# Kernel optimization log

Measured on AMD Instinct MI355X. Metric: run time of the kernel, lower is better.

## Reference

```python
import jax, jax.numpy as jnp
import numpy as np
import math

B, S, D, H = 4, 1024, 512, 8
HD = D // H
HID = 4 * D


def clinear(xr, xi, lm, ph, bm=None, bp=None):
    # magnitude-phase parameterized complex linear: W = exp(lm) * e^{i*ph}
    mag = jnp.exp(lm)
    wr = mag * jnp.cos(ph)
    wi = mag * jnp.sin(ph)
    r = xr @ wr.T - xi @ wi.T
    i = xr @ wi.T + xi @ wr.T
    if bm is not None:
        r = r + bm * jnp.cos(bp)
        i = i + bm * jnp.sin(bp)
    return r, i


def cln(xr, xi, gr, gi, br, bi, eps=1e-6):
    mr = xr.mean(-1, keepdims=True)
    mi = xi.mean(-1, keepdims=True)
    cr, ci = xr - mr, xi - mi
    var = (cr * cr + ci * ci).mean(-1, keepdims=True)
    inv = 1.0 / jnp.sqrt(var + eps)
    nr, ni = cr * inv, ci * inv
    return nr * gr - ni * gi + br, nr * gi + ni * gr + bi


def rotate_half(x):
    h = x.shape[-1] // 2
    return jnp.concatenate([-x[..., h:], x[..., :h]], axis=-1)


def split_heads(x):  # (B,S,D) -> (B,H,S,HD)
    return x.reshape(B, S, H, HD).transpose(0, 2, 1, 3)


def merge_heads(x):  # (B,H,S,HD) -> (B,S,D)
    return x.transpose(0, 2, 1, 3).reshape(B, S, D)


def setup_inputs() -> dict:
    key = jax.random.key(0)
    ks = iter(jax.random.split(key, 64))

    def lin(o_f, i_f):
        lm = jax.random.normal(next(ks), (o_f, i_f)) * 0.1 - 0.5 * math.log(i_f)
        ph = jax.random.uniform(next(ks), (o_f, i_f), minval=-math.pi, maxval=math.pi)
        return lm.astype(jnp.float32), ph.astype(jnp.float32)

    inp = {}
    inp['x_real'] = jax.random.normal(next(ks), (B, S, D), dtype=jnp.float32)
    inp['x_imag'] = jax.random.normal(next(ks), (B, S, D), dtype=jnp.float32)
    inp['ln1_gr'] = jnp.ones(D); inp['ln1_gi'] = jnp.zeros(D)
    inp['ln1_br'] = jnp.zeros(D); inp['ln1_bi'] = jnp.zeros(D)
    for nm in ['q', 'k', 'v', 'o']:
        lm, ph = lin(D, D)
        inp[nm + '_lm'] = lm; inp[nm + '_ph'] = ph
        inp[nm + '_bm'] = jnp.zeros(D); inp[nm + '_bp'] = jnp.zeros(D)
    inp['ln2_gr'] = jnp.ones(D); inp['ln2_gi'] = jnp.zeros(D)
    inp['ln2_br'] = jnp.zeros(D); inp['ln2_bi'] = jnp.zeros(D)
    inp['gate_lm'], inp['gate_ph'] = lin(HID, D)
    inp['up_lm'], inp['up_ph'] = lin(HID, D)
    inp['down_lm'], inp['down_ph'] = lin(D, HID)
    return inp


def reference(x_real, x_imag, ln1_gr, ln1_gi, ln1_br, ln1_bi,
              q_lm, q_ph, q_bm, q_bp, k_lm, k_ph, k_bm, k_bp,
              v_lm, v_ph, v_bm, v_bp, o_lm, o_ph, o_bm, o_bp,
              ln2_gr, ln2_gi, ln2_br, ln2_bi,
              gate_lm, gate_ph, up_lm, up_ph, down_lm, down_ph):
    # --- pre-attention complex LayerNorm ---
    hr, hi = cln(x_real, x_imag, ln1_gr, ln1_gi, ln1_br, ln1_bi)

    # --- complex QKV projections ---
    qr, qi = clinear(hr, hi, q_lm, q_ph, q_bm, q_bp)
    kr, ki = clinear(hr, hi, k_lm, k_ph, k_bm, k_bp)
    vr, vi = clinear(hr, hi, v_lm, v_ph, v_bm, v_bp)
    qr, qi = split_heads(qr), split_heads(qi)
    kr, ki = split_heads(kr), split_heads(ki)
    vr, vi = split_heads(vr), split_heads(vi)

    # --- complex RoPE (same real rotation applied to real & imag parts) ---
    pos = jnp.arange(S, dtype=jnp.float32)
    inv_freq = 1.0 / (10000.0 ** (jnp.arange(0, HD, 2, dtype=jnp.float32) / HD))
    freqs = pos[:, None] * inv_freq[None, :]          # (S, HD/2)
    cos = jnp.concatenate([jnp.cos(freqs)] * 2, -1)[None, None]  # (1,1,S,HD)
    sin = jnp.concatenate([jnp.sin(freqs)] * 2, -1)[None, None]
    rot = lambda x: x * cos + rotate_half(x) * sin
    qr, qi, kr, ki = rot(qr), rot(qi), rot(kr), rot(ki)

    # --- Hermitian attention: Re(q . conj(k)) = qr.kr + qi.ki ---
    scale = 1.0 / math.sqrt(HD)
    scores = (jnp.einsum('bhqd,bhkd->bhqk', qr, kr)
              + jnp.einsum('bhqd,bhkd->bhqk', qi, ki)) * scale
    causal = jnp.tril(jnp.ones((S, S), dtype=bool))
    scores = jnp.where(causal, scores, jnp.float32(-1e9))
    attn = jax.nn.softmax(scores, axis=-1)            # real-valued weights
    ar = jnp.einsum('bhqk,bhkd->bhqd', attn, vr)
    ai = jnp.einsum('bhqk,bhkd->bhqd', attn, vi)
    ar, ai = merge_heads(ar), merge_heads(ai)
    ar, ai = clinear(ar, ai, o_lm, o_ph, o_bm, o_bp)

    # --- residual + LN2 ---
    res_r, res_i = x_real + ar, x_imag + ai
    hr, hi = cln(res_r, res_i, ln2_gr, ln2_gi, ln2_br, ln2_bi)

    # --- complex gated FFN (SwiGLU-style, complex gating) ---
    gr_, gi_ = clinear(hr, hi, gate_lm, gate_ph)
    s = jax.nn.sigmoid(jnp.sqrt(gr_ * gr_ + gi_ * gi_))  # sigmoid(|gate|)
    gar, gai = gr_ * s, gi_ * s
    ur, ui = clinear(hr, hi, up_lm, up_ph)
    hid_r = gar * ur - gai * ui
    hid_i = gar * ui + gai * ur
    dr, di = clinear(hid_r, hid_i, down_lm, down_ph)

    out_r = res_r + dr
    out_i = res_i + di
    return jnp.stack([out_r, out_i], axis=0)  # (2, B, S, D)
```

## Files before the change

kernel.cpp:

```cpp
#include <hip/hip_runtime.h>
#include <math.h>

#define kB 4
#define kS 1024
#define kD 512
#define kH 8
#define kHD 64
#define kHID 2048
#define kNT (kB * kS)
#define kBSD (kNT * kD)

typedef __attribute__((ext_vector_type(8))) short bf16x8;
typedef __attribute__((ext_vector_type(4))) float f32x4;

#define AS1 __attribute__((address_space(1)))
#define AS3 __attribute__((address_space(3)))

__device__ __forceinline__ float bf2f(unsigned short u) {
  return __uint_as_float(((unsigned int)u) << 16);
}
__device__ __forceinline__ unsigned short f2bf(float f) {
  unsigned int u = __float_as_uint(f);
  u += 0x7fffu + ((u >> 16) & 1u);
  return (unsigned short)(u >> 16);
}
__device__ __forceinline__ unsigned int pack2(unsigned short a, unsigned short b) {
  return (unsigned)a | ((unsigned)b << 16);
}

__global__ __launch_bounds__(256) void build_wA_kernel(
    const float* __restrict__ qlm, const float* __restrict__ qph,
    const float* __restrict__ klm, const float* __restrict__ kph,
    const float* __restrict__ vlm, const float* __restrict__ vph,
    const float* __restrict__ olm, const float* __restrict__ oph,
    const float* __restrict__ qbm, const float* __restrict__ qbp,
    const float* __restrict__ kbm, const float* __restrict__ kbp,
    const float* __restrict__ vbm, const float* __restrict__ vbp,
    const float* __restrict__ obm, const float* __restrict__ obp,
    const float* __restrict__ xr, const float* __restrict__ xi,
    const float* __restrict__ g_r, const float* __restrict__ g_i,
    const float* __restrict__ b_r, const float* __restrict__ b_i,
    unsigned short* __restrict__ Wqkv, unsigned short* __restrict__ Wo,
    float* __restrict__ qkvBias, float* __restrict__ oBias,
    unsigned short* __restrict__ H) {
  int bx = blockIdx.x;
  if (bx >= 4104) {
    int w = threadIdx.x >> 6, lane = threadIdx.x & 63;
    int t = (bx - 4104) * 4 + w;
    int d0 = lane * 8;
    const float* xrt = xr + (size_t)t * 512 + d0;
    const float* xit = xi + (size_t)t * 512 + d0;
    float4 a0 = *(const float4*)&xrt[0];
    float4 a1 = *(const float4*)&xrt[4];
    float4 c0 = *(const float4*)&xit[0];
    float4 c1 = *(const float4*)&xit[4];
    float s1 = a0.x + a0.y + a0.z + a0.w + a1.x + a1.y + a1.z + a1.w;
    float s2 = c0.x + c0.y + c0.z + c0.w + c1.x + c1.y + c1.z + c1.w;
#pragma unroll
    for (int off = 1; off < 64; off <<= 1) {
      s1 += __shfl_xor(s1, off);
      s2 += __shfl_xor(s2, off);
    }
    float mr = s1 * (1.f / kD), mi = s2 * (1.f / kD);
    float ar[8] = {a0.x, a0.y, a0.z, a0.w, a1.x, a1.y, a1.z, a1.w};
    float ai[8] = {c0.x, c0.y, c0.z, c0.w, c1.x, c1.y, c1.z, c1.w};
    float v = 0.f;
#pragma unroll
    for (int e = 0; e < 8; e++) {
      float cr = ar[e] - mr, ci = ai[e] - mi;
      v += cr * cr + ci * ci;
    }
#pragma unroll
    for (int off = 1; off < 64; off <<= 1) v += __shfl_xor(v, off);
    float inv = rsqrtf(v * (1.f / kD) + 1e-6f);
    unsigned short pr[8], pi[8];
#pragma unroll
    for (int e = 0; e < 8; e++) {
      float nr = (ar[e] - mr) * inv;
      float ni = (ai[e] - mi) * inv;
      pr[e] = f2bf(nr * g_r[d0 + e] - ni * g_i[d0 + e] + b_r[d0 + e]);
      pi[e] = f2bf(nr * g_i[d0 + e] + ni * g_r[d0 + e] + b_i[d0 + e]);
    }
    unsigned short* ot = H + (size_t)t * 1024 + d0;
    *(bf16x8*)&ot[0] = *(const bf16x8*)pr;
    *(bf16x8*)&ot[512] = *(const bf16x8*)pi;
    return;
  }
  if (bx >= 4096) {
    int gid = (bx - 4096) * 256 + threadIdx.x;
    int seg = gid >> 9, m = gid & 511;
    const float* bm = seg == 0 ? qbm : seg == 1 ? kbm : seg == 2 ? vbm : obm;
    const float* bp = seg == 0 ? qbp : seg == 1 ? kbp : seg == 2 ? vbp : obp;
    float s, c;
    __sincosf(bp[m], &s, &c);
    float br = bm[m] * c, bi = bm[m] * s;
    if (seg < 3) {
      int h = m >> 6, d = m & 63;
      qkvBias[seg * 1024 + h * 128 + d] = br;
      qkvBias[seg * 1024 + h * 128 + 64 + d] = bi;
    } else {
      oBias[m] = br;
      oBias[512 + m] = bi;
    }
    return;
  }
  int gid = bx * 256 + threadIdx.x;
  int seg = gid >> 18;
  int id = gid & 262143;
  const float* lm = seg == 0 ? qlm : seg == 1 ? klm : seg == 2 ? vlm : olm;
  const float* ph = seg == 0 ? qph : seg == 1 ? kph : seg == 2 ? vph : oph;
  float mm = __expf(lm[id]);
  float s, c;
  __sincosf(ph[id], &s, &c);
  float wr = mm * c, wi = mm * s;
  int m = id >> 9, k = id & 511;
  if (seg < 3) {
    int h = m >> 6, d = m & 63;
    size_t rowR = (size_t)seg * 1024 + h * 128 + d;
    size_t rowI = rowR + 64;
    Wqkv[rowR * 1024 + k] = f2bf(wr);
    Wqkv[rowR * 1024 + 512 + k] = f2bf(-wi);
    Wqkv[rowI * 1024 + k] = f2bf(wi);
    Wqkv[rowI * 1024 + 512 + k] = f2bf(wr);
  } else {
    Wo[(size_t)m * 1024 + k] = f2bf(wr);
    Wo[(size_t)m * 1024 + 512 + k] = f2bf(-wi);
    Wo[(size_t)(512 + m) * 1024 + k] = f2bf(wi);
    Wo[(size_t)(512 + m) * 1024 + 512 + k] = f2bf(wr);
  }
}

__global__ __launch_bounds__(256) void build_wB_kernel(
    const float* __restrict__ glm, const float* __restrict__ gph,
    const float* __restrict__ ulm, const float* __restrict__ uph,
    const float* __restrict__ dlm, const float* __restrict__ dph,
    unsigned short* __restrict__ Wgu, unsigned short* __restrict__ Wd) {
  int gid = blockIdx.x * 256 + threadIdx.x;
  int seg = gid >> 19;
  int id0 = (gid & 524287) * 2;
  const float* lm = seg == 0 ? glm : seg == 1 ? ulm : dlm;
  const float* ph = seg == 0 ? gph : seg == 1 ? uph : dph;
  float2 lm2 = *(const float2*)&lm[id0];
  float2 ph2 = *(const float2*)&ph[id0];
  float m0 = __expf(lm2.x), m1 = __expf(lm2.y);
  float s0, c0, s1, c1;
  __sincosf(ph2.x, &s0, &c0);
  __sincosf(ph2.y, &s1, &c1);
  float wr0 = m0 * c0, wi0 = m0 * s0;
  float wr1 = m1 * c1, wi1 = m1 * s1;
  if (seg < 2) {
    int T = id0 >> 9, k = id0 & 511;
    size_t base = (size_t)(T >> 4) * 64 + (T & 15);
    size_t rR = base + (seg * 2 + 0) * 16;
    size_t rI = base + (seg * 2 + 1) * 16;
    *(unsigned int*)&Wgu[rR * 1024 + k] = pack2(f2bf(wr0), f2bf(wr1));
    *(unsigned int*)&Wgu[rR * 1024 + 512 + k] = pack2(f2bf(-wi0), f2bf(-wi1));
    *(unsigned int*)&Wgu[rI * 1024 + k] = pack2(f2bf(wi0), f2bf(wi1));
    *(unsigned int*)&Wgu[rI * 1024 + 512 + k] = pack2(f2bf(wr0), f2bf(wr1));
  } else {
    int m = id0 >> 11, j = id0 & 2047;
    ushort4 a;
    a.x = f2bf(wr0); a.y = f2bf(-wi0); a.z = f2bf(wr1); a.w = f2bf(-wi1);
    *(ushort4*)&Wd[(size_t)m * 4096 + 2 * j] = a;
    ushort4 b;
    b.x = f2bf(wi0); b.y = f2bf(wr0); b.z = f2bf(wi1); b.w = f2bf(wr1);
    *(ushort4*)&Wd[(size_t)(512 + m) * 4096 + 2 * j] = b;
  }
}

__global__ __launch_bounds__(256) void cln_kernel(
    const float* __restrict__ xr, const float* __restrict__ xi, int stride,
    const float* __restrict__ g_r, const float* __restrict__ g_i,
    const float* __restrict__ b_r, const float* __restrict__ b_i,
    unsigned short* __restrict__ out) {
  int w = threadIdx.x >> 6, lane = threadIdx.x & 63;
  int t = blockIdx.x * 4 + w;
  int d0 = lane * 8;
  const float* xrt = xr + (size_t)t * stride + d0;
  const float* xit = xi + (size_t)t * stride + d0;
  float4 a0 = *(const float4*)&xrt[0];
  float4 a1 = *(const float4*)&xrt[4];
  float4 c0 = *(const float4*)&xit[0];
  float4 c1 = *(const float4*)&xit[4];

  float s1 = a0.x + a0.y + a0.z + a0.w + a1.x + a1.y + a1.z + a1.w;
  float s2 = c0.x + c0.y + c0.z + c0.w + c1.x + c1.y + c1.z + c1.w;
#pragma unroll
  for (int off = 1; off < 64; off <<= 1) {
    s1 += __shfl_xor(s1, off);
    s2 += __shfl_xor(s2, off);
  }
  float mr = s1 * (1.f / kD), mi = s2 * (1.f / kD);

  float ar[8] = {a0.x, a0.y, a0.z, a0.w, a1.x, a1.y, a1.z, a1.w};
  float ai[8] = {c0.x, c0.y, c0.z, c0.w, c1.x, c1.y, c1.z, c1.w};
  float v = 0.f;
#pragma unroll
  for (int e = 0; e < 8; e++) {
    float cr = ar[e] - mr, ci = ai[e] - mi;
    v += cr * cr + ci * ci;
  }
#pragma unroll
  for (int off = 1; off < 64; off <<= 1) v += __shfl_xor(v, off);
  float inv = rsqrtf(v * (1.f / kD) + 1e-6f);

  unsigned short pr[8], pi[8];
#pragma unroll
  for (int e = 0; e < 8; e++) {
    float nr = (ar[e] - mr) * inv;
    float ni = (ai[e] - mi) * inv;
    pr[e] = f2bf(nr * g_r[d0 + e] - ni * g_i[d0 + e] + b_r[d0 + e]);
    pi[e] = f2bf(nr * g_i[d0 + e] + ni * g_r[d0 + e] + b_i[d0 + e]);
  }
  unsigned short* ot = out + (size_t)t * 1024 + d0;
  *(bf16x8*)&ot[0] = *(const bf16x8*)pr;
  *(bf16x8*)&ot[512] = *(const bf16x8*)pi;
}

__global__ __launch_bounds__(256) void cgemm_mfma_kernel(
    const unsigned short* __restrict__ X, int ldx,
    const unsigned short* __restrict__ Wt, int K,
    const float* __restrict__ bias, int mode,
    unsigned short* __restrict__ outb, int ldo,
    unsigned short* __restrict__ vtb) {
  __shared__ unsigned short Sh[128 * 64 * 2];
  unsigned short* Xs = Sh;
  unsigned short* Ws = Sh + 8192;

  const int tid = threadIdx.x;
  const int w = tid >> 6;
  const int lane = tid & 63;
  const int quad = lane >> 4;
  const int l15 = lane & 15;
  const int m0 = blockIdx.x * 128;
  const int n0 = blockIdx.y * 128;
  const int wm = (w & 1) * 64;
  const int wn = (w >> 1) * 64;

  const int rsub = lane >> 3;
  const int grow = w * 32 + rsub;
  const int gcol = ((lane & 7) ^ rsub) * 8;
  const unsigned short* gx = X + (size_t)(n0 + grow) * ldx + gcol;
  const unsigned short* gw = Wt + (size_t)(m0 + grow) * K + gcol;

  const int rg = (l15 & 7);

  f32x4 acc[4][4];
#pragma unroll
  for (int i = 0; i < 4; i++)
#pragma unroll
    for (int j = 0; j < 4; j++) acc[i][j] = (f32x4){0.f, 0.f, 0.f, 0.f};

  for (int k0 = 0; k0 < K; k0 += 64) {
    __syncthreads();
#pragma unroll
    for (int t = 0; t < 4; t++) {
      __builtin_amdgcn_global_load_lds((const AS1 void*)(gx + (size_t)t * 8 * ldx + k0),
                                       (AS3 void*)&Xs[w * 2048 + t * 512], 16, 0, 0);
      __builtin_amdgcn_global_load_lds((const AS1 void*)(gw + (size_t)t * 8 * K + k0),
                                       (AS3 void*)&Ws[w * 2048 + t * 512], 16, 0, 0);
    }
    __syncthreads();

#pragma unroll
    for (int ks = 0; ks < 2; ks++) {
      const int gsel = ((ks * 4 + quad) ^ rg) * 8;
      bf16x8 af[4], bf[4];
#pragma unroll
      for (int t = 0; t < 4; t++) {
        af[t] = *(const bf16x8*)&Xs[(wn + t * 16 + l15) * 64 + gsel];
        bf[t] = *(const bf16x8*)&Ws[(wm + t * 16 + l15) * 64 + gsel];
      }
#pragma unroll
      for (int i = 0; i < 4; i++)
#pragma unroll
        for (int j = 0; j < 4; j++)
          acc[i][j] = __builtin_amdgcn_mfma_f32_16x16x32_bf16(af[i], bf[j], acc[i][j], 0, 0, 0);
    }
  }

  if (mode == 4) {
    int T = ((m0 + wm) >> 6) * 16 + l15;
#pragma unroll
    for (int i = 0; i < 4; ++i) {
      int row0 = n0 + wn + i * 16 + quad * 4;
#pragma unroll
      for (int r = 0; r < 4; ++r) {
        float gr = acc[i][0][r], gi = acc[i][1][r];
        float ur = acc[i][2][r], ui = acc[i][3][r];
        float sg = __builtin_amdgcn_rcpf(1.f + __expf(-sqrtf(gr * gr + gi * gi)));
        float gar = gr * sg, gai = gi * sg;
        unsigned int pk = pack2(f2bf(gar * ur - gai * ui), f2bf(gar * ui + gai * ur));
        *(unsigned int*)&outb[(size_t)(row0 + r) * ldo + 2 * T] = pk;
      }
    }
  } else if (mode == 3 && m0 < 2048) {
#pragma unroll
    for (int j = 0; j < 4; ++j) {
      float bv = bias[m0 + wm + j * 16 + l15];
#pragma unroll
      for (int i = 0; i < 4; ++i)
#pragma unroll
        for (int r = 0; r < 4; ++r) acc[i][j][r] += bv;
    }
    const int sbase = ((n0 + wn) & (kS - 1)) + quad * 4;
#pragma unroll
    for (int j01 = 0; j01 < 2; ++j01) {
      float fi = (float)(j01 * 16 + l15);
      float f = __expf(fi * -0.28782313662425572f);
      float c1, s1, c16, s16, cI, sI;
      __sincosf(f, &s1, &c1);
      __sincosf(16.f * f, &s16, &c16);
      __sincosf((float)sbase * f, &sI, &cI);
#pragma unroll
      for (int i = 0; i < 4; ++i) {
        float cc = cI, ss = sI;
#pragma unroll
        for (int r = 0; r < 4; ++r) {
          float x0 = acc[i][j01][r], x1 = acc[i][j01 + 2][r];
          acc[i][j01][r] = x0 * cc - x1 * ss;
          acc[i][j01 + 2][r] = x1 * cc + x0 * ss;
          float cn = cc * c1 - ss * s1;
          ss = ss * c1 + cc * s1;
          cc = cn;
        }
        float cn = cI * c16 - sI * s16;
        sI = sI * c16 + cI * s16;
        cI = cn;
      }
    }
#pragma unroll
    for (int j = 0; j < 4; ++j) {
      int col = m0 + wm + j * 16 + l15;
#pragma unroll
      for (int i = 0; i < 4; ++i) {
        int row0 = n0 + wn + i * 16 + quad * 4;
#pragma unroll
        for (int r = 0; r < 4; ++r)
          outb[(size_t)(row0 + r) * ldo + col] = f2bf(acc[i][j][r]);
      }
    }
  } else {
    unsigned short* Ts = Sh;
#pragma unroll
    for (int p = 0; p < 2; ++p) {
      __syncthreads();
      if ((w & 1) == p) {
#pragma unroll
        for (int j = 0; j < 4; ++j) {
          float bv = bias[m0 + wm + j * 16 + l15];
          int fl = j * 16 + l15;
#pragma unroll
          for (int i = 0; i < 4; ++i) {
            int tk = wn + i * 16 + quad * 4;
#pragma unroll
            for (int r = 0; r < 4; ++r)
              Ts[fl * 130 + tk + r] = f2bf(acc[i][j][r] + bv);
          }
        }
      }
      __syncthreads();
      {
        int fr = tid >> 2, seg = tid & 3;
        int f = (m0 - 2048) + p * 64 + fr;
        int hh = f >> 7, dc = f & 127;
        int bb = n0 >> 10, sbase2 = (n0 & (kS - 1)) + seg * 32;
        unsigned short* dst = &vtb[(size_t)((bb * 8 + hh) * 128 + dc) * 1024 + sbase2];
        const unsigned short* src = &Ts[fr * 130 + seg * 32];
#pragma unroll
        for (int u = 0; u < 4; u++)
          *(bf16x8*)(dst + u * 8) = *(const bf16x8*)(src + u * 8);
      }
    }
  }
}

__global__ __launch_bounds__(256) void cgemm_mfma_n64_kernel(
    const unsigned short* __restrict__ X, int ldx,
    const unsigned short* __restrict__ Wt, int K,
    const float* __restrict__ bias, int mode,
    const float* __restrict__ resr, const float* __restrict__ resi,
    float* __restrict__ outf) {
  __shared__ unsigned short Xs[64 * 128];
  __shared__ unsigned short Ws[128 * 128];

  const int tid = threadIdx.x;
  const int w = tid >> 6;
  const int lane = tid & 63;
  const int quad = lane >> 4;
  const int l15 = lane & 15;
  const int m0 = blockIdx.x * 128;
  const int n0 = blockIdx.y * 64;
  const int wm = (w & 1) * 64;
  const int wn = (w >> 1) * 32;

  f32x4 acc[2][4];
#pragma unroll
  for (int i = 0; i < 2; i++)
#pragma unroll
    for (int j = 0; j < 4; j++) acc[i][j] = (f32x4){0.f, 0.f, 0.f, 0.f};

  for (int k0 = 0; k0 < K; k0 += 128) {
    __syncthreads();
#pragma unroll
    for (int t = 0; t < 4; t++) {
      int key = t * 4 + quad;
      int gc = (l15 ^ key) * 8;
      __builtin_amdgcn_global_load_lds(
          (const AS1 void*)(X + (size_t)(n0 + w * 16 + t * 4 + quad) * ldx + k0 + gc),
          (AS3 void*)&Xs[w * 2048 + t * 512], 16, 0, 0);
    }
#pragma unroll
    for (int t = 0; t < 8; t++) {
      int key = (t * 4 + quad) & 15;
      int gc = (l15 ^ key) * 8;
      __builtin_amdgcn_global_load_lds(
          (const AS1 void*)(Wt + (size_t)(m0 + w * 32 + t * 4 + quad) * K + k0 + gc),
          (AS3 void*)&Ws[w * 4096 + t * 512], 16, 0, 0);
    }
    __syncthreads();

#pragma unroll
    for (int ks = 0; ks < 4; ks++) {
      const int gsel = ((ks * 4 + quad) ^ l15) * 8;
      bf16x8 af[2], bf[4];
#pragma unroll
      for (int t = 0; t < 2; t++)
        af[t] = *(const bf16x8*)&Xs[(wn + t * 16 + l15) * 128 + gsel];
#pragma unroll
      for (int t = 0; t < 4; t++)
        bf[t] = *(const bf16x8*)&Ws[(wm + t * 16 + l15) * 128 + gsel];
#pragma unroll
      for (int i = 0; i < 2; i++)
#pragma unroll
        for (int j = 0; j < 4; j++)
          acc[i][j] = __builtin_amdgcn_mfma_f32_16x16x32_bf16(af[i], bf[j], acc[i][j], 0, 0, 0);
    }
  }

#pragma unroll
  for (int j = 0; j < 4; ++j) {
    int col = m0 + wm + j * 16 + l15;
    float bv = bias ? bias[col] : 0.f;
#pragma unroll
    for (int i = 0; i < 2; ++i) {
      int row0 = n0 + wn + i * 16 + quad * 4;
#pragma unroll
      for (int r = 0; r < 4; ++r) {
        int row = row0 + r;
        float val = acc[i][j][r] + bv;
        if (mode == 1) {
          float xres = (col < 512) ? resr[(size_t)row * 512 + col]
                                   : resi[(size_t)row * 512 + col - 512];
          outf[(size_t)row * 1024 + col] = val + xres;
        } else {
          float rv = resr[(size_t)row * 1024 + col] + val;
          size_t dd = (col < 512) ? ((size_t)row * 512 + col)
                                  : ((size_t)kBSD + (size_t)row * 512 + (col - 512));
          outf[dd] = rv;
        }
      }
    }
  }
}

__global__ __launch_bounds__(256) void attn_mfma_kernel(
    const unsigned short* __restrict__ qkv,
    const unsigned short* __restrict__ vt,
    unsigned short* __restrict__ out) {
  __shared__ unsigned short Ks[64 * 136];
  __shared__ unsigned short Vs[128 * 72];
  __shared__ unsigned short Ps[4 * 16 * 72];

  const int tid = threadIdx.x;
  const int w = tid >> 6;
  const int lane = tid & 63;
  const int quad = lane >> 4;
  const int l15 = lane & 15;

  int bid = blockIdx.x;
  int second = bid >> 8;
  int u = bid & 255;
  int t_ = u & 15;
  const int qt = second ? (15 - t_) : t_;
  const int h = (u >> 4) & 7;
  const int b = second * 2 + (u >> 7);
  const int q0 = qt * 64;
  const int wrow0 = q0 + w * 16;

  bf16x8 qa[4];
  {
    size_t base = (size_t)(b * kS + wrow0 + l15) * 3072 + h * 128;
#pragma unroll
    for (int ks = 0; ks < 4; ks++)
      qa[ks] = *(const bf16x8*)&qkv[base + ks * 32 + quad * 8];
  }

  f32x4 oacc[8];
#pragma unroll
  for (int dt = 0; dt < 8; dt++) oacc[dt] = (f32x4){0.f, 0.f, 0.f, 0.f};
  float m_r[4] = {-1e30f, -1e30f, -1e30f, -1e30f};
  float l_r[4] = {0.f, 0.f, 0.f, 0.f};

  const int nkt = qt + 1;
  const float cexp = 0.1803368801f;

  const unsigned short* gkbase = qkv + 1024 + h * 128;
  const unsigned short* gvbase = vt + (size_t)((b * 8 + h) * 128) * 1024;

  for (int kt = 0; kt < nkt; ++kt) {
    const int k0 = kt * 64;
    __syncthreads();
    {
      const unsigned short* gk = gkbase + (size_t)(b * kS + k0) * 3072;
      int ch = tid * 4;
#pragma unroll
      for (int u2 = 0; u2 < 4; u2++) {
        int r = (ch + u2) >> 4, cc = ((ch + u2) & 15) * 8;
        *(bf16x8*)&Ks[r * 136 + cc] = *(const bf16x8*)&gk[(size_t)r * 3072 + cc];
      }
#pragma unroll
      for (int u2 = 0; u2 < 4; u2++) {
        int vr = (ch + u2) >> 3, vc = ((ch + u2) & 7) * 8;
        *(bf16x8*)&Vs[vr * 72 + vc] = *(const bf16x8*)&gvbase[(size_t)vr * 1024 + k0 + vc];
      }
    }
    __syncthreads();

    f32x4 s[4];
#pragma unroll
    for (int ns = 0; ns < 4; ns++) {
      s[ns] = (f32x4){0.f, 0.f, 0.f, 0.f};
#pragma unroll
      for (int ks = 0; ks < 4; ks++) {
        bf16x8 kb = *(const bf16x8*)&Ks[(ns * 16 + l15) * 136 + ks * 32 + quad * 8];
        s[ns] = __builtin_amdgcn_mfma_f32_16x16x32_bf16(qa[ks], kb, s[ns], 0, 0, 0);
      }
    }

    if (k0 + 63 > wrow0) {
#pragma unroll
      for (int r = 0; r < 4; r++) {
        int qrow = wrow0 + quad * 4 + r;
#pragma unroll
        for (int ns = 0; ns < 4; ns++)
          if (k0 + ns * 16 + l15 > qrow) s[ns][r] = -1e30f;
      }
    }

    float alpha[4];
#pragma unroll
    for (int r = 0; r < 4; r++) {
      float mx = fmaxf(fmaxf(s[0][r], s[1][r]), fmaxf(s[2][r], s[3][r]));
      mx = fmaxf(mx, __shfl_xor(mx, 1));
      mx = fmaxf(mx, __shfl_xor(mx, 2));
      mx = fmaxf(mx, __shfl_xor(mx, 4));
      mx = fmaxf(mx, __shfl_xor(mx, 8));
      float mn = fmaxf(m_r[r], mx);
      float al = exp2f((m_r[r] - mn) * cexp);
      m_r[r] = mn;
      float rs = 0.f;
#pragma unroll
      for (int ns = 0; ns < 4; ns++) {
        float p = exp2f((s[ns][r] - mn) * cexp);
        s[ns][r] = p;
        rs += p;
      }
      rs += __shfl_xor(rs, 1);
      rs += __shfl_xor(rs, 2);
      rs += __shfl_xor(rs, 4);
      rs += __shfl_xor(rs, 8);
      l_r[r] = l_r[r] * al + rs;
      alpha[r] = al;
    }

#pragma unroll
    for (int dt = 0; dt < 8; dt++)
#pragma unroll
      for (int r = 0; r < 4; r++) oacc[dt][r] *= alpha[r];

    unsigned short* pw = &Ps[w * 1152];
#pragma unroll
    for (int r = 0; r < 4; r++) {
      int q = quad * 4 + r;
#pragma unroll
      for (int ns = 0; ns < 4; ns++)
        pw[q * 72 + ns * 16 + l15] = f2bf(s[ns][r]);
    }
    bf16x8 pa0 = *(const bf16x8*)&pw[l15 * 72 + quad * 8];
    bf16x8 pa1 = *(const bf16x8*)&pw[l15 * 72 + 32 + quad * 8];

#pragma unroll
    for (int dt = 0; dt < 8; dt++) {
      bf16x8 vb0 = *(const bf16x8*)&Vs[(dt * 16 + l15) * 72 + quad * 8];
      bf16x8 vb1 = *(const bf16x8*)&Vs[(dt * 16 + l15) * 72 + 32 + quad * 8];
      oacc[dt] = __builtin_amdgcn_mfma_f32_16x16x32_bf16(pa0, vb0, oacc[dt], 0, 0, 0);
      oacc[dt] = __builtin_amdgcn_mfma_f32_16x16x32_bf16(pa1, vb1, oacc[dt], 0, 0, 0);
    }
  }

  float inv[4];
#pragma unroll
  for (int r = 0; r < 4; r++) inv[r] = __builtin_amdgcn_rcpf(l_r[r]);
#pragma unroll
  for (int dt = 0; dt < 8; dt++) {
    int dcat = dt * 16 + l15;
    int col = (dcat < 64) ? (h * 64 + dcat) : (512 + h * 64 + dcat - 64);
#pragma unroll
    for (int r = 0; r < 4; r++) {
      int tok = b * kS + wrow0 + quad * 4 + r;
      out[(size_t)tok * 1024 + col] = f2bf(oacc[dt][r] * inv[r]);
    }
  }
}

extern "C" void kernel_launch(void* const* d_in, const int* in_sizes, int n_in,
                              void* d_out, int out_size, void* d_ws, size_t ws_size,
                              hipStream_t stream) {
  const float* x_real = (const float*)d_in[0];
  const float* x_imag = (const float*)d_in[1];
  const float* ln1_gr = (const float*)d_in[2];
  const float* ln1_gi = (const float*)d_in[3];
  const float* ln1_br = (const float*)d_in[4];
  const float* ln1_bi = (const float*)d_in[5];
  const float* q_lm = (const float*)d_in[6];
  const float* q_ph = (const float*)d_in[7];
  const float* q_bm = (const float*)d_in[8];
  const float* q_bp = (const float*)d_in[9];
  const float* k_lm = (const float*)d_in[10];
  const float* k_ph = (const float*)d_in[11];
  const float* k_bm = (const float*)d_in[12];
  const float* k_bp = (const float*)d_in[13];
  const float* v_lm = (const float*)d_in[14];
  const float* v_ph = (const float*)d_in[15];
  const float* v_bm = (const float*)d_in[16];
  const float* v_bp = (const float*)d_in[17];
  const float* o_lm = (const float*)d_in[18];
  const float* o_ph = (const float*)d_in[19];
  const float* o_bm = (const float*)d_in[20];
  const float* o_bp = (const float*)d_in[21];
  const float* ln2_gr = (const float*)d_in[22];
  const float* ln2_gi = (const float*)d_in[23];
  const float* ln2_br = (const float*)d_in[24];
  const float* ln2_bi = (const float*)d_in[25];
  const float* gate_lm = (const float*)d_in[26];
  const float* gate_ph = (const float*)d_in[27];
  const float* up_lm = (const float*)d_in[28];
  const float* up_ph = (const float*)d_in[29];
  const float* down_lm = (const float*)d_in[30];
  const float* down_ph = (const float*)d_in[31];

  char* wsb = (char*)d_ws;
  unsigned short* Wqkv = (unsigned short*)(wsb + 0);
  unsigned short* Wo   = (unsigned short*)(wsb + 6291456);
  unsigned short* Wgu  = (unsigned short*)(wsb + 8388608);
  unsigned short* Wd   = (unsigned short*)(wsb + 25165824);
  float* qkvBias = (float*)(wsb + 33554432);
  float* oBias   = (float*)(wsb + 33566720);
  float* res     = (float*)(wsb + 33570816);
  unsigned short* H = (unsigned short*)(wsb + 50348032);
  char* big = wsb + 58736640;
  unsigned short* qkv     = (unsigned short*)big;
  unsigned short* attnout = (unsigned short*)(big + 25165824);
  unsigned short* vtb     = (unsigned short*)(big + 33554432);
  unsigned short* hid     = (unsigned short*)big;

  float* outf = (float*)d_out;

  build_wA_kernel<<<5128, 256, 0, stream>>>(q_lm, q_ph, k_lm, k_ph, v_lm, v_ph,
                                            o_lm, o_ph, q_bm, q_bp, k_bm, k_bp,
                                            v_bm, v_bp, o_bm, o_bp,
                                            x_real, x_imag, ln1_gr, ln1_gi,
                                            ln1_br, ln1_bi,
                                            Wqkv, Wo, qkvBias, oBias, H);
  build_wB_kernel<<<6144, 256, 0, stream>>>(gate_lm, gate_ph, up_lm, up_ph,
                                            down_lm, down_ph, Wgu, Wd);

  {
    dim3 g(3072 / 128, kNT / 128);
    cgemm_mfma_kernel<<<g, 256, 0, stream>>>(H, 1024, Wqkv, 1024, qkvBias, 3, qkv, 3072, vtb);
  }

  attn_mfma_kernel<<<kB * kH * (kS / 64), 256, 0, stream>>>(qkv, vtb, attnout);

  {
    dim3 g(1024 / 128, kNT / 64);
    cgemm_mfma_n64_kernel<<<g, 256, 0, stream>>>(attnout, 1024, Wo, 1024, oBias, 1,
                                                 x_real, x_imag, res);
  }

  cln_kernel<<<kNT / 4, 256, 0, stream>>>(res, res + 512, 1024, ln2_gr, ln2_gi, ln2_br, ln2_bi, H);

  {
    dim3 g(8192 / 128, kNT / 128);
    cgemm_mfma_kernel<<<g, 256, 0, stream>>>(H, 1024, Wgu, 1024, nullptr, 4, hid, 4096, nullptr);
  }

  {
    dim3 g(1024 / 128, kNT / 64);
    cgemm_mfma_n64_kernel<<<g, 256, 0, stream>>>(hid, 4096, Wd, 4096, nullptr, 2,
                                                 res, nullptr, outf);
  }
}
```

Measured before the change: 410.5 us.

## Add 256x256-tile gate/up GEMM kernel with direct-to-LDS double buffering

Replaces the 128x128 gate/up complex GEMM launch with a new 512-thread kernel that computes 256x256 output tiles. Global tiles are loaded straight into LDS with global_load_lds into two buffers, and LDS reads use an XOR-swizzled layout. The SwiGLU complex gating epilogue is fused into the kernel and writes packed bf16 output. Larger tiles raise data reuse per byte loaded. In exchange the kernel needs 128 KB of LDS and many accumulator registers, which limits occupancy, and the 512 blocks may balance poorly across CUs.

```diff
diff --git a/kernel.cpp b/kernel.cpp
--- a/kernel.cpp
+++ b/kernel.cpp
@@ -375,6 +375,123 @@
   }
 }
 
+__global__ __launch_bounds__(512, 2) void cgemm_mfma_gu256_kernel(
+    const unsigned short* __restrict__ X, int ldx,
+    const unsigned short* __restrict__ Wt, int K,
+    unsigned short* __restrict__ outb, int ldo) {
+  __shared__ unsigned short Sh[65536];
+
+  const int tid = threadIdx.x;
+  const int w = tid >> 6;
+  const int lane = tid & 63;
+  const int quad = lane >> 4;
+  const int l15 = lane & 15;
+  const int m0 = blockIdx.x * 256;
+  const int n0 = blockIdx.y * 256;
+  const int wfeat = w & 1;
+  const int wtok = w >> 1;
+
+  const int srow = lane >> 3;
+  const int sgran = ((lane & 7) ^ srow) * 8;
+  const unsigned short* gA = X + (size_t)(n0 + w * 32 + srow) * ldx + sgran;
+  const unsigned short* gB = Wt + (size_t)(m0 + w * 32 + srow) * K + sgran;
+
+  f32x4 acc[4][8];
+#pragma unroll
+  for (int i = 0; i < 4; i++)
+#pragma unroll
+    for (int j = 0; j < 8; j++) acc[i][j] = (f32x4){0.f, 0.f, 0.f, 0.f};
+
+  auto stage_tile = [&](int kt, int bsel) {
+    const int k0 = kt * 64;
+    unsigned short* dA = &Sh[bsel * 32768 + w * 2048];
+    unsigned short* dB = &Sh[bsel * 32768 + 16384 + w * 2048];
+#pragma unroll
+    for (int u = 0; u < 4; ++u) {
+      __builtin_amdgcn_global_load_lds((const AS1 void*)(gA + (size_t)u * 8 * ldx + k0),
+                                       (AS3 void*)(dA + u * 512), 16, 0, 0);
+      __builtin_amdgcn_global_load_lds((const AS1 void*)(gB + (size_t)u * 8 * K + k0),
+                                       (AS3 void*)(dB + u * 512), 16, 0, 0);
+    }
+  };
+
+  auto compute_tile = [&](const unsigned short* As, const unsigned short* Bs) {
+    bf16x8 af[4][2];
+#pragma unroll
+    for (int i = 0; i < 4; ++i)
+#pragma unroll
+      for (int ks = 0; ks < 2; ++ks)
+        af[i][ks] = *(const bf16x8*)&As[(wtok * 64 + i * 16 + l15) * 64 +
+                                        (((ks * 4 + quad) ^ (l15 & 7)) * 8)];
+#pragma unroll
+    for (int jp = 0; jp < 4; ++jp) {
+      bf16x8 bq[2][2];
+#pragma unroll
+      for (int jj = 0; jj < 2; ++jj)
+#pragma unroll
+        for (int ks = 0; ks < 2; ++ks)
+          bq[jj][ks] = *(const bf16x8*)&Bs[(wfeat * 128 + (jp * 2 + jj) * 16 + l15) * 64 +
+                                           (((ks * 4 + quad) ^ (l15 & 7)) * 8)];
+      __builtin_amdgcn_s_setprio(1);
+#pragma unroll
+      for (int i = 0; i < 4; ++i)
+#pragma unroll
+        for (int jj = 0; jj < 2; ++jj) {
+          const int j = jp * 2 + jj;
+          acc[i][j] = __builtin_amdgcn_mfma_f32_16x16x32_bf16(af[i][0], bq[jj][0], acc[i][j], 0, 0, 0);
+          acc[i][j] = __builtin_amdgcn_mfma_f32_16x16x32_bf16(af[i][1], bq[jj][1], acc[i][j], 0, 0, 0);
+        }
+      __builtin_amdgcn_s_setprio(0);
+    }
+  };
+
+  const int nt = K >> 6;
+  stage_tile(0, 0);
+  for (int t = 0; t < nt; t += 2) {
+    if (t + 1 < nt) {
+      stage_tile(t + 1, 1);
+      asm volatile("s_waitcnt vmcnt(8)" ::: "memory");
+    } else {
+      asm volatile("s_waitcnt vmcnt(0)" ::: "memory");
+    }
+    __builtin_amdgcn_s_barrier();
+    asm volatile("" ::: "memory");
+    compute_tile(&Sh[0], &Sh[16384]);
+    asm volatile("" ::: "memory");
+    __builtin_amdgcn_s_barrier();
+
+    if (t + 2 < nt) {
+      stage_tile(t + 2, 0);
+      asm volatile("s_waitcnt vmcnt(8)" ::: "memory");
+    } else {
+      asm volatile("s_waitcnt vmcnt(0)" ::: "memory");
+    }
+    __builtin_amdgcn_s_barrier();
+    asm volatile("" ::: "memory");
+    compute_tile(&Sh[32768], &Sh[32768 + 16384]);
+    asm volatile("" ::: "memory");
+    __builtin_amdgcn_s_barrier();
+  }
+
+#pragma unroll
+  for (int i = 0; i < 4; ++i) {
+    int row0 = n0 + wtok * 64 + i * 16 + quad * 4;
+#pragma unroll
+    for (int jh = 0; jh < 2; ++jh) {
+      int T = ((m0 + wfeat * 128 + jh * 64) >> 6) * 16 + l15;
+#pragma unroll
+      for (int r = 0; r < 4; ++r) {
+        float gr = acc[i][jh * 4 + 0][r], gi = acc[i][jh * 4 + 1][r];
+        float ur = acc[i][jh * 4 + 2][r], ui = acc[i][jh * 4 + 3][r];
+        float sg = __builtin_amdgcn_rcpf(1.f + __expf(-sqrtf(gr * gr + gi * gi)));
+        float gar = gr * sg, gai = gi * sg;
+        unsigned int pk = pack2(f2bf(gar * ur - gai * ui), f2bf(gar * ui + gai * ur));
+        *(unsigned int*)&outb[(size_t)(row0 + r) * ldo + 2 * T] = pk;
+      }
+    }
+  }
+}
+
 __global__ __launch_bounds__(256) void cgemm_mfma_n64_kernel(
     const unsigned short* __restrict__ X, int ldx,
     const unsigned short* __restrict__ Wt, int K,
@@ -692,8 +809,8 @@
   cln_kernel<<<kNT / 4, 256, 0, stream>>>(res, res + 512, 1024, ln2_gr, ln2_gi, ln2_br, ln2_bi, H);
 
   {
-    dim3 g(8192 / 128, kNT / 128);
-    cgemm_mfma_kernel<<<g, 256, 0, stream>>>(H, 1024, Wgu, 1024, nullptr, 4, hid, 4096, nullptr);
+    dim3 g(8192 / 256, kNT / 256);
+    cgemm_mfma_gu256_kernel<<<g, 512, 0, stream>>>(H, 1024, Wgu, 1024, hid, 4096);
   }
 
   {
```

After: 392.1 us. -4.5%, faster.
